# Performance work log

Hardware: AMD Instinct MI355X
Metric: run time of the kernel (lower is better)

## Reference

```python
import jax, jax.numpy as jnp
import numpy as np

N = 100000   # nodes
H = 4        # heads
C = 32       # out feats per head (= n_classes)
E = 1600000  # edges
IN = 256     # in feats
NEG_SLOPE = 0.2


def setup_inputs() -> dict:
    key = jax.random.key(0)
    ks = jax.random.split(key, 7)
    x = jax.random.normal(ks[0], (N, IN), dtype=jnp.float32)
    src = jax.random.randint(ks[1], (E,), 0, N, dtype=jnp.int32)
    dst = jax.random.randint(ks[2], (E,), 0, N, dtype=jnp.int32)
    # Xavier-ish scaling for stability
    W = jax.random.normal(ks[3], (IN, H * C), dtype=jnp.float32) / np.sqrt(IN)
    attn_l = jax.random.normal(ks[4], (H, C), dtype=jnp.float32) / np.sqrt(C)
    attn_r = jax.random.normal(ks[5], (H, C), dtype=jnp.float32) / np.sqrt(C)
    bias = jnp.zeros((H * C,), dtype=jnp.float32)
    return {"x": x, "src": src, "dst": dst, "W": W,
            "attn_l": attn_l, "attn_r": attn_r, "bias": bias}


def reference(x, src, dst, W, attn_l, attn_r, bias):
    # GATConv: project, per-edge attention score, edge-softmax over dst, scatter-agg
    feat = (x @ W).reshape(N, H, C)                       # [N,H,C]
    el = jnp.einsum('nhc,hc->nh', feat, attn_l)           # [N,H]
    er = jnp.einsum('nhc,hc->nh', feat, attn_r)           # [N,H]
    e = jax.nn.leaky_relu(el[src] + er[dst], NEG_SLOPE)   # [E,H]
    # numerically-stable segment softmax over incoming edges of each dst node
    m = jax.ops.segment_max(e, dst, num_segments=N)       # [N,H]
    ex = jnp.exp(e - m[dst])                              # [E,H]
    s = jax.ops.segment_sum(ex, dst, num_segments=N)      # [N,H]
    alpha = ex / s[dst]                                   # [E,H]
    # weighted scatter-aggregate of source features
    msg = alpha[:, :, None] * feat[src]                   # [E,H,C]
    out = jax.ops.segment_sum(msg, dst, num_segments=N)   # [N,H,C]
    out = out + bias.reshape(1, H, C)
    h = out.mean(axis=1)                                  # mean over heads -> [N,C]
    return jax.nn.relu(h)
```

## Files before the change

kernel.cpp:

```cpp
#include <hip/hip_runtime.h>
#include <hip/hip_fp16.h>
#include <cstdint>

#define N_NODES 100000
#define H_HEADS 4
#define C_FEATS 32
#define HC 128
#define E_EDGES 1600000
#define IN_F 256
#define NEG_SLOPE 0.2f

#define BSHIFT 7
#define NBUCK 782
#define NREG 8
#define CAPB8 384
#define PH1_CHUNK 4096
#define PH1_BLOCKS ((E_EDGES + PH1_CHUNK - 1) / PH1_CHUNK)
#define GEMM_BLOCKS ((N_NODES + 63) / 64)
#define HALFCAP 1408
#define SWCAP 384

typedef _Float16 half8 __attribute__((ext_vector_type(8)));
typedef _Float16 half4v __attribute__((ext_vector_type(4)));
typedef float f32x4 __attribute__((ext_vector_type(4)));

__global__ __launch_bounds__(256) void prep_w(const float* __restrict__ W,
                                              _Float16* __restrict__ W16t,
                                              int* __restrict__ gcnt) {
    int c = blockIdx.x;
    int k = threadIdx.x;
    W16t[c * IN_F + k] = (_Float16)W[k * HC + c];
    if (c == 0)
        for (int i = k; i < NREG * NBUCK; i += 256) gcnt[i] = 0;
}

__global__ __launch_bounds__(256) void gemm_bucket(const float* __restrict__ x,
                                                   const _Float16* __restrict__ W16t,
                                                   const float* __restrict__ attn_l,
                                                   const float* __restrict__ attn_r,
                                                   const int* __restrict__ src,
                                                   const int* __restrict__ dst,
                                                   _Float16* __restrict__ feat16,
                                                   float* __restrict__ el,
                                                   float* __restrict__ er,
                                                   int* __restrict__ gcnt,
                                                   unsigned* __restrict__ bucket) {
    __shared__ int hist[NBUCK];
    const int t = threadIdx.x;

    if (blockIdx.x < PH1_BLOCKS) {
        const int rg   = blockIdx.x & (NREG - 1);
        const int base = blockIdx.x * PH1_CHUNK;
        const int cnt_e = min(PH1_CHUNK, E_EDGES - base);
        for (int i = t; i < NBUCK; i += 256) hist[i] = 0;
        __syncthreads();

        unsigned w[16]; int bk[16];
        #pragma unroll
        for (int j = 0; j < 16; ++j) {
            int i = t + j * 256;
            bk[j] = -1;
            if (i < cnt_e) {
                int d = dst[base + i];
                int s = src[base + i];
                bk[j] = d >> BSHIFT;
                w[j] = ((unsigned)(d & ((1 << BSHIFT) - 1)) << 24) | (unsigned)s;
                atomicAdd(&hist[bk[j]], 1);
            }
        }
        __syncthreads();
        for (int i = t; i < NBUCK; i += 256) {
            int c = hist[i];
            hist[i] = (c > 0) ? atomicAdd(&gcnt[rg * NBUCK + i], c) : 0;
        }
        __syncthreads();
        #pragma unroll
        for (int j = 0; j < 16; ++j) {
            if (bk[j] >= 0) {
                int slot = atomicAdd(&hist[bk[j]], 1);
                if (slot < CAPB8)
                    bucket[((size_t)rg * NBUCK + bk[j]) * CAPB8 + slot] = w[j];
            }
        }
        return;
    }

    const int blk  = blockIdx.x - PH1_BLOCKS;
    const int w    = t >> 6;
    const int lane = t & 63;
    const int lrow = lane & 15;
    const int kq   = lane >> 4;
    const int gr   = blk * 64 + w * 16 + lrow;
    const int r    = gr < N_NODES ? gr : N_NODES - 1;

    f32x4 acc[8];
    #pragma unroll
    for (int c = 0; c < 8; ++c) acc[c] = (f32x4){0.f, 0.f, 0.f, 0.f};

    #pragma unroll
    for (int s = 0; s < 8; ++s) {
        const int k0 = s * 32 + kq * 8;
        float4 v0 = *(const float4*)&x[(size_t)r * IN_F + k0];
        float4 v1 = *(const float4*)&x[(size_t)r * IN_F + k0 + 4];
        half8 af;
        af[0] = (_Float16)v0.x; af[1] = (_Float16)v0.y;
        af[2] = (_Float16)v0.z; af[3] = (_Float16)v0.w;
        af[4] = (_Float16)v1.x; af[5] = (_Float16)v1.y;
        af[6] = (_Float16)v1.z; af[7] = (_Float16)v1.w;
        #pragma unroll
        for (int c = 0; c < 8; ++c) {
            half8 bf = *(const half8*)&W16t[(size_t)(c * 16 + lrow) * IN_F + k0];
            acc[c] = __builtin_amdgcn_mfma_f32_16x16x32_f16(bf, af, acc[c], 0, 0, 0);
        }
    }

    float pl[4] = {0.f, 0.f, 0.f, 0.f}, pr[4] = {0.f, 0.f, 0.f, 0.f};
    #pragma unroll
    for (int c = 0; c < 8; ++c) {
        const int h = c >> 1;
        #pragma unroll
        for (int j = 0; j < 4; ++j) {
            const int col = c * 16 + kq * 4 + j;
            pl[h] += acc[c][j] * attn_l[col];
            pr[h] += acc[c][j] * attn_r[col];
        }
    }
    #pragma unroll
    for (int h = 0; h < 4; ++h) {
        pl[h] += __shfl_xor(pl[h], 16, 64); pl[h] += __shfl_xor(pl[h], 32, 64);
        pr[h] += __shfl_xor(pr[h], 16, 64); pr[h] += __shfl_xor(pr[h], 32, 64);
    }

    if (gr < N_NODES) {
        #pragma unroll
        for (int c = 0; c < 8; ++c) {
            half4v hv;
            hv[0] = (_Float16)acc[c][0]; hv[1] = (_Float16)acc[c][1];
            hv[2] = (_Float16)acc[c][2]; hv[3] = (_Float16)acc[c][3];
            *(half4v*)&feat16[(size_t)gr * HC + c * 16 + kq * 4] = hv;
        }
        if (kq == 0) {
            *(float4*)&el[gr * 4] = make_float4(pl[0], pl[1], pl[2], pl[3]);
            *(float4*)&er[gr * 4] = make_float4(pr[0], pr[1], pr[2], pr[3]);
        }
    }
}

__global__ __launch_bounds__(256) void gat_gather(const int* __restrict__ gcnt,
                                                  const unsigned* __restrict__ bucket,
                                                  const float* __restrict__ el,
                                                  const float* __restrict__ er,
                                                  const _Float16* __restrict__ feat16,
                                                  const float* __restrict__ bias,
                                                  float* __restrict__ out) {
    __shared__ int   cnt[64];
    __shared__ int   off[64];
    __shared__ int   lcsr[HALFCAP];
    __shared__ float s_w[4][SWCAP][4];

    const int b   = blockIdx.x >> 1;
    const int sub = blockIdx.x & 1;
    const int t   = threadIdx.x;
    const int n0  = (b << BSHIFT) + sub * 64;

    if (t < 64) cnt[t] = 0;
    __syncthreads();
    #pragma unroll
    for (int rr = 0; rr < NREG; ++rr) {
        const int m = min(gcnt[rr * NBUCK + b], CAPB8);
        const size_t rbase = ((size_t)rr * NBUCK + b) * CAPB8;
        for (int i = t; i < m; i += 256) {
            unsigned wrd = bucket[rbase + i];
            int nb = wrd >> 24;
            if ((nb >> 6) == sub) atomicAdd(&cnt[nb & 63], 1);
        }
    }
    __syncthreads();
    if (t < 64) {
        int v = cnt[t];
        int inc = v;
        #pragma unroll
        for (int o = 1; o < 64; o <<= 1) {
            int u = __shfl_up(inc, o, 64);
            if (t >= o) inc += u;
        }
        off[t] = inc - v;
        cnt[t] = 0;
    }
    __syncthreads();
    #pragma unroll
    for (int rr = 0; rr < NREG; ++rr) {
        const int m = min(gcnt[rr * NBUCK + b], CAPB8);
        const size_t rbase = ((size_t)rr * NBUCK + b) * CAPB8;
        for (int i = t; i < m; i += 256) {
            unsigned wrd = bucket[rbase + i];
            int nb = wrd >> 24;
            if ((nb >> 6) == sub) {
                int r = atomicAdd(&cnt[nb & 63], 1);
                int p = off[nb & 63] + r;
                if (p < HALFCAP) lcsr[p] = (int)(wrd & 0xBFFFFFFFu);
            }
        }
    }
    __syncthreads();

    const int wv   = t >> 6;
    const int lane = t & 63;
    const int q    = lane >> 4;
    const int ql   = lane & 15;
    const int h    = ql >> 2;

    const int wbase = off[wv * 16];
    const int wlast = wv * 16 + 15;
    const int nE    = min(off[wlast] + cnt[wlast] - wbase, SWCAP);
    for (int i = lane; i < nE; i += 64) {
        int wrd = lcsr[wbase + i];
        int s   = wrd & 0xFFFFFF;
        int nl  = (wrd >> 24) & 63;
        float4 a  = *(const float4*)&el[(size_t)s * 4];
        float4 bb = *(const float4*)&er[(size_t)(n0 + nl) * 4];
        float v0 = a.x + bb.x, v1 = a.y + bb.y, v2 = a.z + bb.z, v3 = a.w + bb.w;
        v0 = fmaxf(v0, NEG_SLOPE * v0); v1 = fmaxf(v1, NEG_SLOPE * v1);
        v2 = fmaxf(v2, NEG_SLOPE * v2); v3 = fmaxf(v3, NEG_SLOPE * v3);
        float4 w4;
        w4.x = __expf(v0); w4.y = __expf(v1); w4.z = __expf(v2); w4.w = __expf(v3);
        *(float4*)&s_w[wv][i][0] = w4;
    }
    __builtin_amdgcn_sched_barrier(0);

    float bv[8];
    #pragma unroll
    for (int k = 0; k < 8; ++k) bv[k] = bias[h * C_FEATS + (ql & 3) * 8 + k];

    for (int r0 = 0; r0 < 16; r0 += 4) {
        const int nl   = wv * 16 + r0 + q;
        const int n    = n0 + nl;
        const int bofs = off[nl];
        const int widx = bofs - wbase;
        int dg = cnt[nl];
        dg = min(dg, SWCAP - widx);
        if (dg < 0 || n >= N_NODES) dg = 0;

        float ac[8] = {0.f, 0.f, 0.f, 0.f, 0.f, 0.f, 0.f, 0.f};
        float sh = 0.f;
        #pragma unroll 4
        for (int j = 0; j < dg; ++j) {
            float wgt = s_w[wv][widx + j][h];
            int s = lcsr[bofs + j] & 0xFFFFFF;
            half8 f = *(const half8*)&feat16[(size_t)s * HC + ql * 8];
            #pragma unroll
            for (int k = 0; k < 8; ++k) ac[k] += wgt * (float)f[k];
            if ((ql & 3) == 0) sh += wgt;
        }
        __builtin_amdgcn_sched_barrier(0);

        float d = __shfl(sh, (lane & 48) | (ql & 12), 64);
        float inv = d > 0.f ? 1.f / d : 0.f;
        float o[8];
        #pragma unroll
        for (int k = 0; k < 8; ++k) o[k] = ac[k] * inv + bv[k];
        #pragma unroll
        for (int k = 0; k < 8; ++k) {
            o[k] += __shfl_xor(o[k], 4, 64);
            o[k] += __shfl_xor(o[k], 8, 64);
        }
        if (n < N_NODES && ql < 4) {
            float4 r1, r2;
            r1.x = fmaxf(o[0] * 0.25f, 0.f); r1.y = fmaxf(o[1] * 0.25f, 0.f);
            r1.z = fmaxf(o[2] * 0.25f, 0.f); r1.w = fmaxf(o[3] * 0.25f, 0.f);
            r2.x = fmaxf(o[4] * 0.25f, 0.f); r2.y = fmaxf(o[5] * 0.25f, 0.f);
            r2.z = fmaxf(o[6] * 0.25f, 0.f); r2.w = fmaxf(o[7] * 0.25f, 0.f);
            *(float4*)&out[(size_t)n * C_FEATS + ql * 8]     = r1;
            *(float4*)&out[(size_t)n * C_FEATS + ql * 8 + 4] = r2;
        }
    }
}

extern "C" void kernel_launch(void* const* d_in, const int* in_sizes, int n_in,
                              void* d_out, int out_size, void* d_ws, size_t ws_size,
                              hipStream_t stream) {
    const float* x      = (const float*)d_in[0];
    const int*   src    = (const int*)d_in[1];
    const int*   dst    = (const int*)d_in[2];
    const float* W      = (const float*)d_in[3];
    const float* attn_l = (const float*)d_in[4];
    const float* attn_r = (const float*)d_in[5];
    const float* bias   = (const float*)d_in[6];
    float* out = (float*)d_out;

    char* ws = (char*)d_ws;
    const size_t FEAT16_B = (size_t)N_NODES * HC * 2;
    const size_t NH_B     = (size_t)N_NODES * H_HEADS * 4;
    size_t off = 0;
    _Float16* feat16 = (_Float16*)(ws + off); off += FEAT16_B;
    float* el        = (float*)(ws + off);    off += NH_B;
    float* er        = (float*)(ws + off);    off += NH_B;
    _Float16* W16t   = (_Float16*)(ws + off); off += (size_t)HC * IN_F * 2;
    int*   gcnt      = (int*)(ws + off);      off += (size_t)NREG * NBUCK * 4;
    off = (off + 255) & ~(size_t)255;
    unsigned* bucket = (unsigned*)(ws + off); off += (size_t)NREG * NBUCK * CAPB8 * 4;

    prep_w<<<HC, IN_F, 0, stream>>>(W, W16t, gcnt);
    gemm_bucket<<<PH1_BLOCKS + GEMM_BLOCKS, 256, 0, stream>>>(
        x, W16t, attn_l, attn_r, src, dst, feat16, el, er, gcnt, bucket);
    gat_gather<<<NBUCK * 2, 256, 0, stream>>>(gcnt, bucket, el, er,
                                              feat16, bias, out);
}
```

Measured before the change: 164.6 us.

## Drop shared histogram in edge bucketing and double GEMM rows per wave

The edge-bucketing phase no longer builds a per-block LDS histogram and reserves ranges. Each edge now does a direct global atomicAdd on its bucket counter, and src/dst are read with vectorized nontemporal 4-wide loads. The GEMM phase now has each wave compute two 16-row tiles, so every W16t fragment load is reused across two MFMAs, and GEMM_BLOCKS is halved. Occupancy is hinted with launch_bounds(256,4). The per-edge global atomics greatly increase atomic traffic and contention, and the order of slots within a bucket becomes nondeterministic.

```diff
diff --git a/kernel.cpp b/kernel.cpp
--- a/kernel.cpp
+++ b/kernel.cpp
@@ -16,13 +16,14 @@
 #define CAPB8 384
 #define PH1_CHUNK 4096
 #define PH1_BLOCKS ((E_EDGES + PH1_CHUNK - 1) / PH1_CHUNK)
-#define GEMM_BLOCKS ((N_NODES + 63) / 64)
+#define GEMM_BLOCKS ((N_NODES + 127) / 128)
 #define HALFCAP 1408
 #define SWCAP 384
 
 typedef _Float16 half8 __attribute__((ext_vector_type(8)));
 typedef _Float16 half4v __attribute__((ext_vector_type(4)));
 typedef float f32x4 __attribute__((ext_vector_type(4)));
+typedef int i32x4 __attribute__((ext_vector_type(4)));
 
 __global__ __launch_bounds__(256) void prep_w(const float* __restrict__ W,
                                               _Float16* __restrict__ W16t,
@@ -34,52 +35,51 @@
         for (int i = k; i < NREG * NBUCK; i += 256) gcnt[i] = 0;
 }
 
-__global__ __launch_bounds__(256) void gemm_bucket(const float* __restrict__ x,
-                                                   const _Float16* __restrict__ W16t,
-                                                   const float* __restrict__ attn_l,
-                                                   const float* __restrict__ attn_r,
-                                                   const int* __restrict__ src,
-                                                   const int* __restrict__ dst,
-                                                   _Float16* __restrict__ feat16,
-                                                   float* __restrict__ el,
-                                                   float* __restrict__ er,
-                                                   int* __restrict__ gcnt,
-                                                   unsigned* __restrict__ bucket) {
-    __shared__ int hist[NBUCK];
+__global__ __launch_bounds__(256, 4) void gemm_bucket(const float* __restrict__ x,
+                                                      const _Float16* __restrict__ W16t,
+                                                      const float* __restrict__ attn_l,
+                                                      const float* __restrict__ attn_r,
+                                                      const int* __restrict__ src,
+                                                      const int* __restrict__ dst,
+                                                      _Float16* __restrict__ feat16,
+                                                      float* __restrict__ el,
+                                                      float* __restrict__ er,
+                                                      int* __restrict__ gcnt,
+                                                      unsigned* __restrict__ bucket) {
     const int t = threadIdx.x;
 
     if (blockIdx.x < PH1_BLOCKS) {
-        const int rg   = blockIdx.x & (NREG - 1);
-        const int base = blockIdx.x * PH1_CHUNK;
+        const int rg    = blockIdx.x & (NREG - 1);
+        const int base  = blockIdx.x * PH1_CHUNK;
         const int cnt_e = min(PH1_CHUNK, E_EDGES - base);
-        for (int i = t; i < NBUCK; i += 256) hist[i] = 0;
-        __syncthreads();
-
-        unsigned w[16]; int bk[16];
-        #pragma unroll
-        for (int j = 0; j < 16; ++j) {
-            int i = t + j * 256;
-            bk[j] = -1;
-            if (i < cnt_e) {
-                int d = dst[base + i];
-                int s = src[base + i];
-                bk[j] = d >> BSHIFT;
-                w[j] = ((unsigned)(d & ((1 << BSHIFT) - 1)) << 24) | (unsigned)s;
-                atomicAdd(&hist[bk[j]], 1);
-            }
-        }
-        __syncthreads();
-        for (int i = t; i < NBUCK; i += 256) {
-            int c = hist[i];
-            hist[i] = (c > 0) ? atomicAdd(&gcnt[rg * NBUCK + i], c) : 0;
-        }
-        __syncthreads();
-        #pragma unroll
-        for (int j = 0; j < 16; ++j) {
-            if (bk[j] >= 0) {
-                int slot = atomicAdd(&hist[bk[j]], 1);
-                if (slot < CAPB8)
-                    bucket[((size_t)rg * NBUCK + bk[j]) * CAPB8 + slot] = w[j];
+        const i32x4* d4 = (const i32x4*)(dst + base);
+        const i32x4* s4 = (const i32x4*)(src + base);
+        #pragma unroll
+        for (int j = 0; j < 4; ++j) {
+            int idx = t + j * 256;
+            int e0  = idx * 4;
+            if (e0 + 3 < cnt_e) {
+                i32x4 d = __builtin_nontemporal_load(&d4[idx]);
+                i32x4 s = __builtin_nontemporal_load(&s4[idx]);
+                #pragma unroll
+                for (int k = 0; k < 4; ++k) {
+                    int dj = d[k];
+                    int bk = dj >> BSHIFT;
+                    unsigned w = ((unsigned)(dj & ((1 << BSHIFT) - 1)) << 24) | (unsigned)s[k];
+                    int slot = atomicAdd(&gcnt[rg * NBUCK + bk], 1);
+                    if (slot < CAPB8)
+                        bucket[((size_t)rg * NBUCK + bk) * CAPB8 + slot] = w;
+                }
+            } else if (e0 < cnt_e) {
+                for (int k = 0; k < 4 && e0 + k < cnt_e; ++k) {
+                    int dj = dst[base + e0 + k];
+                    int sj = src[base + e0 + k];
+                    int bk = dj >> BSHIFT;
+                    unsigned w = ((unsigned)(dj & ((1 << BSHIFT) - 1)) << 24) | (unsigned)sj;
+                    int slot = atomicAdd(&gcnt[rg * NBUCK + bk], 1);
+                    if (slot < CAPB8)
+                        bucket[((size_t)rg * NBUCK + bk) * CAPB8 + slot] = w;
+                }
             }
         }
         return;
@@ -90,58 +90,74 @@
     const int lane = t & 63;
     const int lrow = lane & 15;
     const int kq   = lane >> 4;
-    const int gr   = blk * 64 + w * 16 + lrow;
-    const int r    = gr < N_NODES ? gr : N_NODES - 1;
-
-    f32x4 acc[8];
-    #pragma unroll
-    for (int c = 0; c < 8; ++c) acc[c] = (f32x4){0.f, 0.f, 0.f, 0.f};
+    const int gr0  = blk * 128 + w * 32 + lrow;
+    const int gr1  = gr0 + 16;
+    const int r0   = gr0 < N_NODES ? gr0 : N_NODES - 1;
+    const int r1   = gr1 < N_NODES ? gr1 : N_NODES - 1;
+
+    f32x4 acc0[8], acc1[8];
+    #pragma unroll
+    for (int c = 0; c < 8; ++c) {
+        acc0[c] = (f32x4){0.f, 0.f, 0.f, 0.f};
+        acc1[c] = (f32x4){0.f, 0.f, 0.f, 0.f};
+    }
 
     #pragma unroll
     for (int s = 0; s < 8; ++s) {
         const int k0 = s * 32 + kq * 8;
-        float4 v0 = *(const float4*)&x[(size_t)r * IN_F + k0];
-        float4 v1 = *(const float4*)&x[(size_t)r * IN_F + k0 + 4];
-        half8 af;
-        af[0] = (_Float16)v0.x; af[1] = (_Float16)v0.y;
-        af[2] = (_Float16)v0.z; af[3] = (_Float16)v0.w;
-        af[4] = (_Float16)v1.x; af[5] = (_Float16)v1.y;
-        af[6] = (_Float16)v1.z; af[7] = (_Float16)v1.w;
+        float4 u0 = *(const float4*)&x[(size_t)r0 * IN_F + k0];
+        float4 u1 = *(const float4*)&x[(size_t)r0 * IN_F + k0 + 4];
+        float4 v0 = *(const float4*)&x[(size_t)r1 * IN_F + k0];
+        float4 v1 = *(const float4*)&x[(size_t)r1 * IN_F + k0 + 4];
+        half8 af0, af1;
+        af0[0] = (_Float16)u0.x; af0[1] = (_Float16)u0.y;
+        af0[2] = (_Float16)u0.z; af0[3] = (_Float16)u0.w;
+        af0[4] = (_Float16)u1.x; af0[5] = (_Float16)u1.y;
+        af0[6] = (_Float16)u1.z; af0[7] = (_Float16)u1.w;
+        af1[0] = (_Float16)v0.x; af1[1] = (_Float16)v0.y;
+        af1[2] = (_Float16)v0.z; af1[3] = (_Float16)v0.w;
+        af1[4] = (_Float16)v1.x; af1[5] = (_Float16)v1.y;
+        af1[6] = (_Float16)v1.z; af1[7] = (_Float16)v1.w;
         #pragma unroll
         for (int c = 0; c < 8; ++c) {
             half8 bf = *(const half8*)&W16t[(size_t)(c * 16 + lrow) * IN_F + k0];
-            acc[c] = __builtin_amdgcn_mfma_f32_16x16x32_f16(bf, af, acc[c], 0, 0, 0);
-        }
-    }
-
-    float pl[4] = {0.f, 0.f, 0.f, 0.f}, pr[4] = {0.f, 0.f, 0.f, 0.f};
-    #pragma unroll
-    for (int c = 0; c < 8; ++c) {
-        const int h = c >> 1;
-        #pragma unroll
-        for (int j = 0; j < 4; ++j) {
-            const int col = c * 16 + kq * 4 + j;
-            pl[h] += acc[c][j] * attn_l[col];
-            pr[h] += acc[c][j] * attn_r[col];
-        }
-    }
-    #pragma unroll
-    for (int h = 0; h < 4; ++h) {
-        pl[h] += __shfl_xor(pl[h], 16, 64); pl[h] += __shfl_xor(pl[h], 32, 64);
-        pr[h] += __shfl_xor(pr[h], 16, 64); pr[h] += __shfl_xor(pr[h], 32, 64);
-    }
-
-    if (gr < N_NODES) {
+            acc0[c] = __builtin_amdgcn_mfma_f32_16x16x32_f16(bf, af0, acc0[c], 0, 0, 0);
+            acc1[c] = __builtin_amdgcn_mfma_f32_16x16x32_f16(bf, af1, acc1[c], 0, 0, 0);
+        }
+    }
+
+    #pragma unroll
+    for (int tile = 0; tile < 2; ++tile) {
+        const int gr = tile == 0 ? gr0 : gr1;
+        f32x4* acc = tile == 0 ? acc0 : acc1;
+        float pl[4] = {0.f, 0.f, 0.f, 0.f}, pr[4] = {0.f, 0.f, 0.f, 0.f};
         #pragma unroll
         for (int c = 0; c < 8; ++c) {
-            half4v hv;
-            hv[0] = (_Float16)acc[c][0]; hv[1] = (_Float16)acc[c][1];
-            hv[2] = (_Float16)acc[c][2]; hv[3] = (_Float16)acc[c][3];
-            *(half4v*)&feat16[(size_t)gr * HC + c * 16 + kq * 4] = hv;
-        }
-        if (kq == 0) {
-            *(float4*)&el[gr * 4] = make_float4(pl[0], pl[1], pl[2], pl[3]);
-            *(float4*)&er[gr * 4] = make_float4(pr[0], pr[1], pr[2], pr[3]);
+            const int h = c >> 1;
+            #pragma unroll
+            for (int j = 0; j < 4; ++j) {
+                const int col = c * 16 + kq * 4 + j;
+                pl[h] += acc[c][j] * attn_l[col];
+                pr[h] += acc[c][j] * attn_r[col];
+            }
+        }
+        #pragma unroll
+        for (int h = 0; h < 4; ++h) {
+            pl[h] += __shfl_xor(pl[h], 16, 64); pl[h] += __shfl_xor(pl[h], 32, 64);
+            pr[h] += __shfl_xor(pr[h], 16, 64); pr[h] += __shfl_xor(pr[h], 32, 64);
+        }
+        if (gr < N_NODES) {
+            #pragma unroll
+            for (int c = 0; c < 8; ++c) {
+                half4v hv;
+                hv[0] = (_Float16)acc[c][0]; hv[1] = (_Float16)acc[c][1];
+                hv[2] = (_Float16)acc[c][2]; hv[3] = (_Float16)acc[c][3];
+                *(half4v*)&feat16[(size_t)gr * HC + c * 16 + kq * 4] = hv;
+            }
+            if (kq == 0) {
+                *(float4*)&el[gr * 4] = make_float4(pl[0], pl[1], pl[2], pl[3]);
+                *(float4*)&er[gr * 4] = make_float4(pr[0], pr[1], pr[2], pr[3]);
+            }
         }
     }
 }
```

Measured after the change: 219.3 us. 1.33x slower.
